# Kernel optimization log

Hardware: AMD Instinct MI355X
Metric: run time of the kernel (lower is better)

## Reference

```python
import jax, jax.numpy as jnp
import numpy as np

J, F_ = 17, 32  # joints x per-joint features; C = J*F_ = 544
H = 8           # num_heads
EPS = 1e-5


def _layernorm(x, g, b):
    mu = jnp.mean(x, axis=-1, keepdims=True)
    var = jnp.mean((x - mu) ** 2, axis=-1, keepdims=True)
    return (x - mu) * jax.lax.rsqrt(var + EPS) * g + b


def setup_inputs() -> dict:
    key = jax.random.key(0)
    ks = jax.random.split(key, 8)
    B, N, C = 8, 1024, J * F_
    x = jax.random.normal(ks[0], (B, N, C), dtype=jnp.float32)
    s = 1.0 / np.sqrt(C)
    return {
        "x": x,
        "norm_g": jnp.ones((F_,), jnp.float32),
        "norm_b": jnp.zeros((F_,), jnp.float32),
        "ap_w": jax.random.normal(ks[1], (1, F_), jnp.float32) / np.sqrt(F_),
        "ap_b": jnp.zeros((1,), jnp.float32),
        "norm2_g": jnp.ones((C,), jnp.float32),
        "norm2_b": jnp.zeros((C,), jnp.float32),
        "qkv_w": jax.random.normal(ks[2], (3 * C, C), jnp.float32) * s,
        "proj_w": jax.random.normal(ks[3], (C, C), jnp.float32) * s,
        "proj_b": jnp.zeros((C,), jnp.float32),
        "scaling_factor": jnp.array([2.0], jnp.float32),
    }


def reference(x, norm_g, norm_b, ap_w, ap_b, norm2_g, norm2_b, qkv_w, proj_w, proj_b, scaling_factor):
    B, N, C = x.shape
    hd = C // H
    # --- attention pooling over joints ---
    xr = x.reshape(B, N, J, F_)
    xr = _layernorm(xr, norm_g, norm_b)                      # [B,N,17,32]
    scores = jnp.einsum('bnjf,of->bnjo', xr, ap_w)[..., 0] + ap_b[0]  # [B,N,17]
    # nn.Softmax(dim=1): softmax over sequence axis N (faithful to source)
    w = jax.nn.softmax(scores, axis=1)
    xp = (xr * w[..., None]).reshape(B, N, C)
    xp = _layernorm(xp, norm2_g, norm2_b)
    # --- position-scaled self-attention ---
    positions = jnp.linspace(0.0, 1.0, N, dtype=jnp.float32)  # [N]
    pos_scale = jnp.exp(-scaling_factor[0] * (positions - 0.5) ** 2)  # per-key scale
    qkv = (xp @ qkv_w.T).reshape(B, N, 3, H, hd)
    q = qkv[:, :, 0].transpose(0, 2, 1, 3)  # [B,H,N,hd]
    k = qkv[:, :, 1].transpose(0, 2, 1, 3)
    v = qkv[:, :, 2].transpose(0, 2, 1, 3)
    scale = hd ** -0.5
    attn = jnp.einsum('bhqd,bhkd->bhqk', q, k) * (scale * pos_scale[None, None, None, :])
    attn = jax.nn.softmax(attn, axis=-1)
    out = jnp.einsum('bhqk,bhkd->bhqd', attn, v)
    out = out.transpose(0, 2, 1, 3).reshape(B, N, C)
    return out @ proj_w.T + proj_b
```

## Files before the change

### kernel.cpp

```cpp
#include <hip/hip_runtime.h>
#include <hip/hip_bf16.h>

#define BB 8
#define NN 1024
#define CC 544
#define JJ 17
#define FF 32
#define HH 8
#define HD 68
#define BN 8192
#define KD 544
#define NCQ 1632
#define NCQP 1664
#define NCPP 640
#define HDP 96
#define AQR 64

using f32x4  = __attribute__((ext_vector_type(4))) float;
using bf16x8 = __attribute__((ext_vector_type(8))) short;

__device__ __forceinline__ void gld_lds16(const void* g, void* l) {
  __builtin_amdgcn_global_load_lds(
      (const __attribute__((address_space(1))) void*)g,
      (__attribute__((address_space(3))) void*)l, 16, 0, 0);
}

__global__ __launch_bounds__(256) void wconv(const float* __restrict__ qkv_w,
                                             const float* __restrict__ proj_w,
                                             __hip_bfloat16* __restrict__ qw,
                                             __hip_bfloat16* __restrict__ pw,
                                             char* __restrict__ qkp) {
  int idx = blockIdx.x * 256 + threadIdx.x;
  const int t1 = NCQP * KD;
  const int t2 = t1 + NCPP * KD;
  if (idx < t1) {
    int r = idx / KD;
    qw[idx] = __float2bfloat16(r < NCQ ? qkv_w[idx] : 0.f);
  } else if (idx < t2) {
    int k = idx - t1;
    int r = k / KD;
    pw[k] = __float2bfloat16(r < CC ? proj_w[k] : 0.f);
  } else {
    int k = idx - t2;
    if (k < 131072 * 7) {
      int row = k / 7, i = k - row * 7;
      *(unsigned long long*)(qkp + (size_t)row * 192 + 136 + i * 8) = 0ull;
    }
  }
}

__global__ __launch_bounds__(64) void ln1_scores(const float* __restrict__ x,
                                                 const float* __restrict__ g,
                                                 const float* __restrict__ bta,
                                                 const float* __restrict__ apw,
                                                 const float* __restrict__ apb,
                                                 float* __restrict__ xr,
                                                 float* __restrict__ scores) {
  int bn = blockIdx.x, lane = threadIdx.x;
  int f = lane & 31, half = lane >> 5;
  const float* row = x + (size_t)bn * CC;
  float gg = g[f], bb = bta[f], aw = apw[f], ab = apb[0];
  for (int it = 0; it < 9; ++it) {
    int j = it * 2 + half;
    bool act = (j < JJ);
    float v = act ? row[j * FF + f] : 0.f;
    float s = v;
    for (int m = 16; m >= 1; m >>= 1) s += __shfl_xor(s, m);
    float mu = s * (1.f / 32.f);
    float dv = v - mu;
    float s2 = dv * dv;
    for (int m = 16; m >= 1; m >>= 1) s2 += __shfl_xor(s2, m);
    float xn = dv * rsqrtf(s2 * (1.f / 32.f) + 1e-5f) * gg + bb;
    float sc = xn * aw;
    for (int m = 16; m >= 1; m >>= 1) sc += __shfl_xor(sc, m);
    if (act) {
      xr[(size_t)bn * CC + j * FF + f] = xn;
      if (f == 0) scores[bn * JJ + j] = sc + ab;
    }
  }
}

__global__ __launch_bounds__(256) void softmax_n(const float* __restrict__ scores,
                                                 float* __restrict__ wsm) {
  int bj = blockIdx.x;
  int b = bj / JJ, j = bj - b * JJ;
  const float* s = scores + (size_t)b * NN * JJ + j;
  float* wp = wsm + (size_t)b * NN * JJ + j;
  int t = threadIdx.x;
  float v[4];
  float mx = -1e30f;
#pragma unroll
  for (int i = 0; i < 4; ++i) { v[i] = s[(t + 256 * i) * JJ]; mx = fmaxf(mx, v[i]); }
#pragma unroll
  for (int m = 32; m >= 1; m >>= 1) mx = fmaxf(mx, __shfl_xor(mx, m));
  __shared__ float red[4];
  if ((t & 63) == 0) red[t >> 6] = mx;
  __syncthreads();
  mx = fmaxf(fmaxf(red[0], red[1]), fmaxf(red[2], red[3]));
  float sum = 0.f;
#pragma unroll
  for (int i = 0; i < 4; ++i) { v[i] = __expf(v[i] - mx); sum += v[i]; }
#pragma unroll
  for (int m = 32; m >= 1; m >>= 1) sum += __shfl_xor(sum, m);
  __shared__ float red2[4];
  if ((t & 63) == 0) red2[t >> 6] = sum;
  __syncthreads();
  sum = red2[0] + red2[1] + red2[2] + red2[3];
  float inv = 1.f / sum;
#pragma unroll
  for (int i = 0; i < 4; ++i) wp[(t + 256 * i) * JJ] = v[i] * inv;
}

__global__ __launch_bounds__(64) void ln2_xp(const float* __restrict__ xr,
                                             const float* __restrict__ wsm,
                                             const float* __restrict__ g2,
                                             const float* __restrict__ b2,
                                             __hip_bfloat16* __restrict__ xp) {
  int bn = blockIdx.x, lane = threadIdx.x;
  __shared__ float wsh[JJ];
  if (lane < JJ) wsh[lane] = wsm[bn * JJ + lane];
  __syncthreads();
  float vals[9];
  float sum = 0.f;
  for (int it = 0; it < 9; ++it) {
    int c = it * 64 + lane;
    float v = 0.f;
    if (c < CC) v = xr[(size_t)bn * CC + c] * wsh[c >> 5];
    vals[it] = v;
    sum += v;
  }
  for (int m = 32; m >= 1; m >>= 1) sum += __shfl_xor(sum, m);
  float mu = sum * (1.f / 544.f);
  float s2 = 0.f;
  for (int it = 0; it < 9; ++it) {
    int c = it * 64 + lane;
    if (c < CC) { float dv = vals[it] - mu; s2 += dv * dv; }
  }
  for (int m = 32; m >= 1; m >>= 1) s2 += __shfl_xor(s2, m);
  float rstd = rsqrtf(s2 * (1.f / 544.f) + 1e-5f);
  for (int it = 0; it < 9; ++it) {
    int c = it * 64 + lane;
    if (c < CC)
      xp[(size_t)bn * CC + c] = __float2bfloat16((vals[it] - mu) * rstd * g2[c] + b2[c]);
  }
}

template <int MODE>
__global__ __launch_bounds__(256) void gemm_nt(const __hip_bfloat16* __restrict__ A,
                                               const __hip_bfloat16* __restrict__ Bw,
                                               __hip_bfloat16* __restrict__ Qp,
                                               __hip_bfloat16* __restrict__ Kp,
                                               __hip_bfloat16* __restrict__ Vt,
                                               float* __restrict__ Cf,
                                               const float* __restrict__ bias,
                                               const float* __restrict__ sfp) {
  __shared__ __hip_bfloat16 As[128 * 32];
  __shared__ __hip_bfloat16 Bs[128 * 32];
  const int t = threadIdx.x;
  const int w = t >> 6, lane = t & 63;
  const int fr = lane & 15, fq = lane >> 4;
  const int m0 = blockIdx.x * 128;
  const int n0 = blockIdx.y * 128;
  const int wm = (w >> 1) * 64, wn = (w & 1) * 64;

  f32x4 acc[4][4] = {};

  const __hip_bfloat16* Ag = A + (size_t)m0 * KD;
  const __hip_bfloat16* Bg = Bw + (size_t)n0 * KD;

  for (int kt = 0; kt < 17; ++kt) {
    const int k0 = kt * 32;
#pragma unroll
    for (int i = 0; i < 2; ++i) {
      int cb = (i * 4 + w) * 64;
      int chunk = cb + lane;
      int row = chunk >> 2, c16 = chunk & 3;
      gld_lds16(Ag + (size_t)row * KD + k0 + c16 * 8, &As[cb * 8]);
      gld_lds16(Bg + (size_t)row * KD + k0 + c16 * 8, &Bs[cb * 8]);
    }
    __syncthreads();
    bf16x8 af[4], bfr[4];
#pragma unroll
    for (int tm = 0; tm < 4; ++tm)
      af[tm] = *(const bf16x8*)&As[(wm + tm * 16 + fr) * 32 + fq * 8];
#pragma unroll
    for (int tn = 0; tn < 4; ++tn)
      bfr[tn] = *(const bf16x8*)&Bs[(wn + tn * 16 + fr) * 32 + fq * 8];
#pragma unroll
    for (int tm = 0; tm < 4; ++tm)
#pragma unroll
      for (int tn = 0; tn < 4; ++tn)
        acc[tm][tn] = __builtin_amdgcn_mfma_f32_16x16x32_bf16(af[tm], bfr[tn], acc[tm][tn], 0, 0, 0);
    __syncthreads();
  }

  if (MODE == 1) {
#pragma unroll
    for (int tn = 0; tn < 4; ++tn) {
      int o = n0 + wn + tn * 16 + fr;
      if (o < CC) {
        float bb = bias[o];
#pragma unroll
        for (int tm = 0; tm < 4; ++tm) {
          int m = m0 + wm + tm * 16 + fq * 4;
#pragma unroll
          for (int r = 0; r < 4; ++r)
            Cf[(size_t)(m + r) * CC + o] = acc[tm][tn][r] + bb;
        }
      }
    }
  } else {
    int b = m0 >> 10;
    float sf = sfp[0];
#pragma unroll
    for (int tn = 0; tn < 4; ++tn) {
      int o = n0 + wn + tn * 16 + fr;
      if (o < 2 * CC) {
        bool is_k = (o >= CC);
        int oo = is_k ? o - CC : o;
        int h = oo / HD;
        int d = oo - h * HD;
        __hip_bfloat16* base = is_k ? Kp : Qp;
        __hip_bfloat16* dst = base + ((size_t)(b * HH + h) * NN) * HDP + d;
#pragma unroll
        for (int tm = 0; tm < 4; ++tm) {
          int m = m0 + wm + tm * 16 + fq * 4;
          int n = m & (NN - 1);
#pragma unroll
          for (int r = 0; r < 4; ++r) {
            float v = acc[tm][tn][r];
            if (is_k) {
              float pos = (n + r) * (1.f / 1023.f) - 0.5f;
              v *= __expf(-sf * pos * pos) * 0.12126781251816650f;
            }
            dst[(size_t)(n + r) * HDP] = __float2bfloat16(v);
          }
        }
      } else if (o < NCQ) {
        int oo = o - 2 * CC;
        int h = oo / HD;
        int d = oo - h * HD;
        __hip_bfloat16* vrow = Vt + (((size_t)b * HH + h) * HD + d) * NN;
#pragma unroll
        for (int tm = 0; tm < 4; ++tm) {
          int m = m0 + wm + tm * 16 + fq * 4;
          int n = m & (NN - 1);
#pragma unroll
          for (int r = 0; r < 4; ++r)
            vrow[n + r] = __float2bfloat16(acc[tm][tn][r]);
        }
      }
    }
  }
}

__global__ __launch_bounds__(128) void attn_kernel(const __hip_bfloat16* __restrict__ Qp,
                                                   const __hip_bfloat16* __restrict__ Kp,
                                                   const __hip_bfloat16* __restrict__ Vt,
                                                   __hip_bfloat16* __restrict__ Ao) {
  __shared__ __hip_bfloat16 Qs[12 * 64 * 8];
  __shared__ __hip_bfloat16 Ks[2][12 * 64 * 8];
  const int t = threadIdx.x;
  const int w = t >> 6, lane = t & 63;
  const int fr = lane & 15, fq = lane >> 4;
  const int idx = blockIdx.x;
  const int bh = idx & 63, qt = idx >> 6;
  const int h = bh & 7, b = bh >> 3;

  const __hip_bfloat16* qtile = Qp + ((size_t)bh * NN + qt * AQR) * HDP;
  const __hip_bfloat16* kbase = Kp + (size_t)bh * NN * HDP;
  const __hip_bfloat16* vbase = Vt + (size_t)bh * HD * NN;

#pragma unroll
  for (int i = 0; i < 6; ++i) {
    int kb = i * 2 + w;
    gld_lds16(qtile + (size_t)lane * HDP + kb * 8, &Qs[kb * 64 * 8]);
  }
#pragma unroll
  for (int i = 0; i < 6; ++i) {
    int kb = i * 2 + w;
    gld_lds16(kbase + (size_t)lane * HDP + kb * 8, &Ks[0][kb * 64 * 8]);
  }
  __syncthreads();
  bf16x8 qa[2][3];
#pragma unroll
  for (int g = 0; g < 2; ++g)
#pragma unroll
    for (int ks = 0; ks < 3; ++ks)
      qa[g][ks] = *(const bf16x8*)&Qs[((ks * 4 + fq) * 64 + w * 32 + g * 16 + fr) * 8];
  __syncthreads();

  f32x4 o_acc[2][5] = {};
  float l_part[2][4] = {};
  const int dclamp = (fr < 4) ? 0 : 1;

  for (int kt = 0; kt < 16; ++kt) {
    const int cur = kt & 1;
    bf16x8 vfrag[5][2];
#pragma unroll
    for (int tv = 0; tv < 5; ++tv) {
      int d = tv * 16 + fr;
      int dc = (tv == 4 && dclamp) ? 0 : d;
#pragma unroll
      for (int ks2 = 0; ks2 < 2; ++ks2)
        vfrag[tv][ks2] = *(const bf16x8*)(vbase + (size_t)dc * NN + kt * 64 + ks2 * 32 + fq * 8);
    }
    if (kt < 15) {
      const __hip_bfloat16* ktile = kbase + (size_t)(kt + 1) * 64 * HDP;
#pragma unroll
      for (int i = 0; i < 6; ++i) {
        int kb = i * 2 + w;
        gld_lds16(ktile + (size_t)lane * HDP + kb * 8, &Ks[1 - cur][kb * 64 * 8]);
      }
    }

    f32x4 s[2][4] = {};
#pragma unroll
    for (int tn = 0; tn < 4; ++tn) {
#pragma unroll
      for (int ks = 0; ks < 3; ++ks) {
        bf16x8 kb = *(const bf16x8*)&Ks[cur][((ks * 4 + fq) * 64 + tn * 16 + fr) * 8];
        s[0][tn] = __builtin_amdgcn_mfma_f32_16x16x32_bf16(qa[0][ks], kb, s[0][tn], 0, 0, 0);
        s[1][tn] = __builtin_amdgcn_mfma_f32_16x16x32_bf16(qa[1][ks], kb, s[1][tn], 0, 0, 0);
      }
    }
#pragma unroll
    for (int g = 0; g < 2; ++g) {
      __hip_bfloat16* Ps = &Qs[(w * 2 + g) * 1152];
#pragma unroll
      for (int tn = 0; tn < 4; ++tn)
#pragma unroll
        for (int r = 0; r < 4; ++r) {
          float p = __expf(s[g][tn][r]);
          l_part[g][r] += p;
          Ps[(fq * 4 + r) * 72 + tn * 16 + fr] = __float2bfloat16(p);
        }
    }
#pragma unroll
    for (int ks2 = 0; ks2 < 2; ++ks2) {
      bf16x8 pa0 = *(const bf16x8*)&Qs[(w * 2 + 0) * 1152 + fr * 72 + ks2 * 32 + fq * 8];
      bf16x8 pa1 = *(const bf16x8*)&Qs[(w * 2 + 1) * 1152 + fr * 72 + ks2 * 32 + fq * 8];
#pragma unroll
      for (int tv = 0; tv < 5; ++tv) {
        o_acc[0][tv] = __builtin_amdgcn_mfma_f32_16x16x32_bf16(pa0, vfrag[tv][ks2], o_acc[0][tv], 0, 0, 0);
        o_acc[1][tv] = __builtin_amdgcn_mfma_f32_16x16x32_bf16(pa1, vfrag[tv][ks2], o_acc[1][tv], 0, 0, 0);
      }
    }
    __syncthreads();
  }
#pragma unroll
  for (int g = 0; g < 2; ++g) {
    __hip_bfloat16* obase = Ao + (size_t)(b * NN + qt * AQR + w * 32 + g * 16) * CC + h * HD;
    float inv[4];
#pragma unroll
    for (int r = 0; r < 4; ++r) {
      float l = l_part[g][r];
#pragma unroll
      for (int msk = 8; msk >= 1; msk >>= 1) l += __shfl_xor(l, msk);
      inv[r] = 1.f / l;
    }
#pragma unroll
    for (int tv = 0; tv < 5; ++tv) {
      int d = tv * 16 + fr;
      if (d < HD) {
#pragma unroll
        for (int r = 0; r < 4; ++r)
          obase[(size_t)(fq * 4 + r) * CC + d] = __float2bfloat16(o_acc[g][tv][r] * inv[r]);
      }
    }
  }
}

extern "C" void kernel_launch(void* const* d_in, const int* in_sizes, int n_in,
                              void* d_out, int out_size, void* d_ws, size_t ws_size,
                              hipStream_t stream) {
  (void)in_sizes; (void)n_in; (void)out_size; (void)ws_size;
  const float* x       = (const float*)d_in[0];
  const float* norm_g  = (const float*)d_in[1];
  const float* norm_b  = (const float*)d_in[2];
  const float* ap_w    = (const float*)d_in[3];
  const float* ap_b    = (const float*)d_in[4];
  const float* norm2_g = (const float*)d_in[5];
  const float* norm2_b = (const float*)d_in[6];
  const float* qkv_w   = (const float*)d_in[7];
  const float* proj_w  = (const float*)d_in[8];
  const float* proj_b  = (const float*)d_in[9];
  const float* sf      = (const float*)d_in[10];
  float* out = (float*)d_out;
  char* ws = (char*)d_ws;

  float* xr              = (float*)(ws);
  float* scores          = (float*)(ws + 17825792);
  float* wsm             = (float*)(ws + 18382848);
  __hip_bfloat16* xp     = (__hip_bfloat16*)(ws + 18939904);
  __hip_bfloat16* qw     = (__hip_bfloat16*)(ws + 27852800);
  __hip_bfloat16* pw     = (__hip_bfloat16*)(ws + 29663232);
  __hip_bfloat16* vt     = (__hip_bfloat16*)(ws + 30359552);
  __hip_bfloat16* ao     = (__hip_bfloat16*)(ws + 39272448);
  __hip_bfloat16* qp     = (__hip_bfloat16*)(ws + 48185344);
  __hip_bfloat16* kp     = (__hip_bfloat16*)(ws + 60768256);

  wconv<<<8480, 256, 0, stream>>>(qkv_w, proj_w, qw, pw, (char*)qp);
  ln1_scores<<<BN, 64, 0, stream>>>(x, norm_g, norm_b, ap_w, ap_b, xr, scores);
  softmax_n<<<BB * JJ, 256, 0, stream>>>(scores, wsm);
  ln2_xp<<<BN, 64, 0, stream>>>(xr, wsm, norm2_g, norm2_b, xp);
  gemm_nt<0><<<dim3(64, 13), 256, 0, stream>>>(xp, qw, qp, kp, vt, nullptr, nullptr, sf);
  attn_kernel<<<dim3((NN / AQR) * HH * BB), 128, 0, stream>>>(qp, kp, vt, ao);
  gemm_nt<1><<<dim3(64, 5), 256, 0, stream>>>(ao, pw, nullptr, nullptr, nullptr, out, proj_b, nullptr);
}
```

Baseline: 226.2 us.

## Split attention query tile across four waves instead of two

The attention kernel now runs 256 threads per block with four waves, each handling 16 query rows instead of 32. The K and Q tile loads are spread across the four waves, and per-wave accumulators shrink from two row groups to one. This cuts register pressure and raises wave-level parallelism and occupancy (launch bounds 256,4). In exchange, each V fragment is loaded by twice as many waves, so per-FLOP global V traffic and LDS K reads go up.

After: 254.9 us. +12.7%, slower.

```diff
diff --git a/kernel.cpp b/kernel.cpp
--- a/kernel.cpp
+++ b/kernel.cpp
@@ -254,10 +254,10 @@
   }
 }
 
-__global__ __launch_bounds__(128) void attn_kernel(const __hip_bfloat16* __restrict__ Qp,
-                                                   const __hip_bfloat16* __restrict__ Kp,
-                                                   const __hip_bfloat16* __restrict__ Vt,
-                                                   __hip_bfloat16* __restrict__ Ao) {
+__global__ __launch_bounds__(256, 4) void attn_kernel(const __hip_bfloat16* __restrict__ Qp,
+                                                      const __hip_bfloat16* __restrict__ Kp,
+                                                      const __hip_bfloat16* __restrict__ Vt,
+                                                      __hip_bfloat16* __restrict__ Ao) {
   __shared__ __hip_bfloat16 Qs[12 * 64 * 8];
   __shared__ __hip_bfloat16 Ks[2][12 * 64 * 8];
   const int t = threadIdx.x;
@@ -272,26 +272,24 @@
   const __hip_bfloat16* vbase = Vt + (size_t)bh * HD * NN;
 
 #pragma unroll
-  for (int i = 0; i < 6; ++i) {
-    int kb = i * 2 + w;
+  for (int i = 0; i < 3; ++i) {
+    int kb = i * 4 + w;
     gld_lds16(qtile + (size_t)lane * HDP + kb * 8, &Qs[kb * 64 * 8]);
   }
 #pragma unroll
-  for (int i = 0; i < 6; ++i) {
-    int kb = i * 2 + w;
+  for (int i = 0; i < 3; ++i) {
+    int kb = i * 4 + w;
     gld_lds16(kbase + (size_t)lane * HDP + kb * 8, &Ks[0][kb * 64 * 8]);
   }
   __syncthreads();
-  bf16x8 qa[2][3];
-#pragma unroll
-  for (int g = 0; g < 2; ++g)
-#pragma unroll
-    for (int ks = 0; ks < 3; ++ks)
-      qa[g][ks] = *(const bf16x8*)&Qs[((ks * 4 + fq) * 64 + w * 32 + g * 16 + fr) * 8];
-  __syncthreads();
-
-  f32x4 o_acc[2][5] = {};
-  float l_part[2][4] = {};
+  bf16x8 qa[3];
+#pragma unroll
+  for (int ks = 0; ks < 3; ++ks)
+    qa[ks] = *(const bf16x8*)&Qs[((ks * 4 + fq) * 64 + w * 16 + fr) * 8];
+  __syncthreads();
+
+  f32x4 o_acc[5] = {};
+  float l_part[4] = {};
   const int dclamp = (fr < 4) ? 0 : 1;
 
   for (int kt = 0; kt < 16; ++kt) {
@@ -308,65 +306,55 @@
     if (kt < 15) {
       const __hip_bfloat16* ktile = kbase + (size_t)(kt + 1) * 64 * HDP;
 #pragma unroll
-      for (int i = 0; i < 6; ++i) {
-        int kb = i * 2 + w;
+      for (int i = 0; i < 3; ++i) {
+        int kb = i * 4 + w;
         gld_lds16(ktile + (size_t)lane * HDP + kb * 8, &Ks[1 - cur][kb * 64 * 8]);
       }
     }
 
-    f32x4 s[2][4] = {};
+    f32x4 s[4] = {};
 #pragma unroll
     for (int tn = 0; tn < 4; ++tn) {
 #pragma unroll
       for (int ks = 0; ks < 3; ++ks) {
         bf16x8 kb = *(const bf16x8*)&Ks[cur][((ks * 4 + fq) * 64 + tn * 16 + fr) * 8];
-        s[0][tn] = __builtin_amdgcn_mfma_f32_16x16x32_bf16(qa[0][ks], kb, s[0][tn], 0, 0, 0);
-        s[1][tn] = __builtin_amdgcn_mfma_f32_16x16x32_bf16(qa[1][ks], kb, s[1][tn], 0, 0, 0);
-      }
-    }
-#pragma unroll
-    for (int g = 0; g < 2; ++g) {
-      __hip_bfloat16* Ps = &Qs[(w * 2 + g) * 1152];
-#pragma unroll
-      for (int tn = 0; tn < 4; ++tn)
-#pragma unroll
-        for (int r = 0; r < 4; ++r) {
-          float p = __expf(s[g][tn][r]);
-          l_part[g][r] += p;
-          Ps[(fq * 4 + r) * 72 + tn * 16 + fr] = __float2bfloat16(p);
-        }
-    }
+        s[tn] = __builtin_amdgcn_mfma_f32_16x16x32_bf16(qa[ks], kb, s[tn], 0, 0, 0);
+      }
+    }
+    __hip_bfloat16* Ps = &Qs[w * 1152];
+#pragma unroll
+    for (int tn = 0; tn < 4; ++tn)
+#pragma unroll
+      for (int r = 0; r < 4; ++r) {
+        float p = __expf(s[tn][r]);
+        l_part[r] += p;
+        Ps[(fq * 4 + r) * 72 + tn * 16 + fr] = __float2bfloat16(p);
+      }
 #pragma unroll
     for (int ks2 = 0; ks2 < 2; ++ks2) {
-      bf16x8 pa0 = *(const bf16x8*)&Qs[(w * 2 + 0) * 1152 + fr * 72 + ks2 * 32 + fq * 8];
-      bf16x8 pa1 = *(const bf16x8*)&Qs[(w * 2 + 1) * 1152 + fr * 72 + ks2 * 32 + fq * 8];
-#pragma unroll
-      for (int tv = 0; tv < 5; ++tv) {
-        o_acc[0][tv] = __builtin_amdgcn_mfma_f32_16x16x32_bf16(pa0, vfrag[tv][ks2], o_acc[0][tv], 0, 0, 0);
-        o_acc[1][tv] = __builtin_amdgcn_mfma_f32_16x16x32_bf16(pa1, vfrag[tv][ks2], o_acc[1][tv], 0, 0, 0);
-      }
+      bf16x8 pa = *(const bf16x8*)&Qs[w * 1152 + fr * 72 + ks2 * 32 + fq * 8];
+#pragma unroll
+      for (int tv = 0; tv < 5; ++tv)
+        o_acc[tv] = __builtin_amdgcn_mfma_f32_16x16x32_bf16(pa, vfrag[tv][ks2], o_acc[tv], 0, 0, 0);
     }
     __syncthreads();
   }
-#pragma unroll
-  for (int g = 0; g < 2; ++g) {
-    __hip_bfloat16* obase = Ao + (size_t)(b * NN + qt * AQR + w * 32 + g * 16) * CC + h * HD;
-    float inv[4];
-#pragma unroll
-    for (int r = 0; r < 4; ++r) {
-      float l = l_part[g][r];
-#pragma unroll
-      for (int msk = 8; msk >= 1; msk >>= 1) l += __shfl_xor(l, msk);
-      inv[r] = 1.f / l;
-    }
-#pragma unroll
-    for (int tv = 0; tv < 5; ++tv) {
-      int d = tv * 16 + fr;
-      if (d < HD) {
-#pragma unroll
-        for (int r = 0; r < 4; ++r)
-          obase[(size_t)(fq * 4 + r) * CC + d] = __float2bfloat16(o_acc[g][tv][r] * inv[r]);
-      }
+  __hip_bfloat16* obase = Ao + (size_t)(b * NN + qt * AQR + w * 16) * CC + h * HD;
+  float inv[4];
+#pragma unroll
+  for (int r = 0; r < 4; ++r) {
+    float l = l_part[r];
+#pragma unroll
+    for (int msk = 8; msk >= 1; msk >>= 1) l += __shfl_xor(l, msk);
+    inv[r] = 1.f / l;
+  }
+#pragma unroll
+  for (int tv = 0; tv < 5; ++tv) {
+    int d = tv * 16 + fr;
+    if (d < HD) {
+#pragma unroll
+      for (int r = 0; r < 4; ++r)
+        obase[(size_t)(fq * 4 + r) * CC + d] = __float2bfloat16(o_acc[tv][r] * inv[r]);
     }
   }
 }
@@ -405,6 +393,6 @@
   softmax_n<<<BB * JJ, 256, 0, stream>>>(scores, wsm);
   ln2_xp<<<BN, 64, 0, stream>>>(xr, wsm, norm2_g, norm2_b, xp);
   gemm_nt<0><<<dim3(64, 13), 256, 0, stream>>>(xp, qw, qp, kp, vt, nullptr, nullptr, sf);
-  attn_kernel<<<dim3((NN / AQR) * HH * BB), 128, 0, stream>>>(qp, kp, vt, ao);
+  attn_kernel<<<dim3((NN / AQR) * HH * BB), 256, 0, stream>>>(qp, kp, vt, ao);
   gemm_nt<1><<<dim3(64, 5), 256, 0, stream>>>(ao, pw, nullptr, nullptr, nullptr, out, proj_b, nullptr);
 }
```
